# Optimization experiments

Measured on AMD Instinct MI355X. Metric: run time of the kernel, lower is better.

Reference implementation:

```python
import jax, jax.numpy as jnp
import numpy as np


def setup_inputs() -> dict:
    key = jax.random.key(0)
    k1, _ = jax.random.split(key)
    N = 4096
    states = jax.random.normal(k1, (N, 8), dtype=jnp.float32)
    log_tau = jnp.log(jnp.asarray(0.05, dtype=jnp.float32))
    return {"states": states, "log_tau": log_tau}


def reference(states, log_tau):
    N = states.shape[0]
    tau = jnp.exp(log_tau)
    pos = (states[:, :2] + states[:, 2:4]) / 2.0   # [N, 2]
    vel = (states[:, 4:6] + states[:, 6:8]) / 2.0  # [N, 2]
    dpos = pos[:, None, :] - pos[None, :, :]       # [N, N, 2]
    dvel = vel[:, None, :] - vel[None, :, :]       # [N, N, 2]
    f_ij = jnp.concatenate([dpos, dvel], axis=-1)  # [N, N, 4]
    dist = jnp.sqrt(jnp.sum(dpos ** 2, axis=-1) + 1e-08)  # [N, N]
    eye = jnp.eye(N, dtype=bool)
    logits = jnp.where(eye, -1e9, -dist / tau)
    alpha = jax.nn.softmax(logits, axis=-1)        # [N, N]
    mu = jnp.einsum('ij,ijd->id', alpha, f_ij)     # [N, 4]
    diff2 = (f_ij - mu[:, None, :]) ** 2           # [N, N, 4]
    sigma = jnp.sqrt(jnp.einsum('ij,ijd->id', alpha, diff2) + 1e-06)  # [N, 4]
    group_vel = jnp.broadcast_to(jnp.mean(vel, axis=0, keepdims=True), (N, 2))
    vel_dev = vel - group_vel
    return jnp.concatenate([mu, sigma, group_vel, vel_dev], axis=-1)  # [N, 12]
```

## Files before the change

### kernel.cpp

```cpp
#include <hip/hip_runtime.h>
#include <math.h>

typedef float v2f __attribute__((ext_vector_type(2)));

#define N_PTS 4096
#define BLOCK 512
#define RPB 4
#define SLICES (BLOCK / RPB)
#define JPS (N_PTS / SLICES)

__global__ __launch_bounds__(BLOCK, 4) void fused_kernel(
        const float* __restrict__ states,
        const float* __restrict__ log_tau_p,
        float* __restrict__ out) {
    __shared__ float4 pv[N_PTS];
    __shared__ float wsum[8][2];
    __shared__ float red[8][RPB][10];

    const int tid  = threadIdx.x;
    const int lane = tid & 63;
    const int wave = tid >> 6;

    const float c = -__expf(-log_tau_p[0]) * 1.4426950408889634f;

    float svx = 0.f, svy = 0.f;
    #pragma unroll
    for (int k = 0; k < N_PTS / BLOCK; ++k) {
        const int p = tid + k * BLOCK;
        const float4 s0 = *reinterpret_cast<const float4*>(states + p * 8);
        const float4 s1 = *reinterpret_cast<const float4*>(states + p * 8 + 4);
        float4 e;
        e.x = (s0.x + s0.z) * 0.5f;
        e.y = (s0.y + s0.w) * 0.5f;
        e.z = (s1.x + s1.z) * 0.5f;
        e.w = (s1.y + s1.w) * 0.5f;
        pv[p] = e;
        svx += e.z; svy += e.w;
    }
    #pragma unroll
    for (int off = 32; off; off >>= 1) {
        svx += __shfl_down(svx, off);
        svy += __shfl_down(svy, off);
    }
    if (lane == 0) { wsum[wave][0] = svx; wsum[wave][1] = svy; }
    __syncthreads();

    const int rowg  = blockIdx.x * RPB + (lane & 3);
    const int slice = wave * (SLICES / 8) + (lane >> 2);
    const float4 pi = pv[rowg];

    float l = 0.f;
    v2f S1p = {0.f, 0.f}, S1v = {0.f, 0.f}, S2p = {0.f, 0.f}, S2v = {0.f, 0.f};

    #pragma unroll 8
    for (int tt = 0; tt < JPS; ++tt) {
        const float4 q = pv[slice + tt * SLICES];
        v2f dp = {pi.x - q.x, pi.y - q.y};
        v2f dv = {pi.z - q.z, pi.w - q.w};
        v2f p2 = dp * dp;
        float d2 = p2.x + p2.y + 1e-8f;
        float dist = __builtin_amdgcn_sqrtf(d2);
        float w = __builtin_amdgcn_exp2f(dist * c);
        l += w;
        v2f wv = {w, w};
        S1p += dp * wv;
        S1v += dv * wv;
        S2p += p2 * wv;
        S2v += (dv * dv) * wv;
    }

    #pragma unroll
    for (int off = 4; off < 64; off <<= 1) {
        l     += __shfl_xor(l, off);
        S1p.x += __shfl_xor(S1p.x, off);
        S1p.y += __shfl_xor(S1p.y, off);
        S1v.x += __shfl_xor(S1v.x, off);
        S1v.y += __shfl_xor(S1v.y, off);
        S2p.x += __shfl_xor(S2p.x, off);
        S2p.y += __shfl_xor(S2p.y, off);
        S2v.x += __shfl_xor(S2v.x, off);
        S2v.y += __shfl_xor(S2v.y, off);
    }
    if (lane < RPB) {
        float* rr = red[wave][lane];
        rr[0] = l;
        rr[1] = S1p.x; rr[2] = S1p.y; rr[3] = S1v.x; rr[4] = S1v.y;
        rr[5] = S2p.x; rr[6] = S2p.y; rr[7] = S2v.x; rr[8] = S2v.y;
    }
    __syncthreads();

    if (tid < RPB) {
        float acc[9];
        #pragma unroll
        for (int cc = 0; cc < 9; ++cc) acc[cc] = red[0][tid][cc];
        #pragma unroll
        for (int wv = 1; wv < 8; ++wv)
            #pragma unroll
            for (int cc = 0; cc < 9; ++cc) acc[cc] += red[wv][tid][cc];

        const float w_diag = __builtin_amdgcn_exp2f(__builtin_amdgcn_sqrtf(1e-8f) * c);
        const float inv_l = 1.0f / (acc[0] - w_diag);

        float gvx = 0.f, gvy = 0.f;
        #pragma unroll
        for (int wv = 0; wv < 8; ++wv) { gvx += wsum[wv][0]; gvy += wsum[wv][1]; }
        gvx *= (1.0f / N_PTS);
        gvy *= (1.0f / N_PTS);

        const int row = blockIdx.x * RPB + tid;
        const float4 pr = pv[row];

        float mu[4], sg[4];
        #pragma unroll
        for (int d = 0; d < 4; ++d) mu[d] = acc[1 + d] * inv_l;
        #pragma unroll
        for (int d = 0; d < 4; ++d) {
            float v = fmaf(-mu[d], mu[d], acc[5 + d] * inv_l);
            sg[d] = __builtin_amdgcn_sqrtf(v + 1e-6f);
        }
        float4* o = reinterpret_cast<float4*>(out + row * 12);
        o[0] = make_float4(mu[0], mu[1], mu[2], mu[3]);
        o[1] = make_float4(sg[0], sg[1], sg[2], sg[3]);
        o[2] = make_float4(gvx, gvy, pr.z - gvx, pr.w - gvy);
    }
}

extern "C" void kernel_launch(void* const* d_in, const int* in_sizes, int n_in,
                              void* d_out, int out_size, void* d_ws, size_t ws_size,
                              hipStream_t stream) {
    const float* states  = (const float*)d_in[0];
    const float* log_tau = (const float*)d_in[1];
    float* out = (float*)d_out;
    fused_kernel<<<N_PTS / RPB, BLOCK, 0, stream>>>(states, log_tau, out);
}
```

Before: 69.99 us.

## Stage points in two LDS chunks and prescale positions to cut per-pair ops

Shared memory is halved by loading the point table in two 2048-point chunks with a sync between passes, and launch bounds rise from 4 to 6 blocks per CU to allow more resident blocks. Positions are prescaled by 1/tau*log2e so the inner loop drops the multiply before exp2. The squared terms now reuse the weighted products, and the results are rescaled once at the end. This adds extra barriers and a second staging pass per block, and it changes rounding slightly.

```diff
diff --git a/kernel.cpp b/kernel.cpp
--- a/kernel.cpp
+++ b/kernel.cpp
@@ -6,14 +6,16 @@
 #define N_PTS 4096
 #define BLOCK 512
 #define RPB 4
+#define CHUNK 2048
 #define SLICES (BLOCK / RPB)
-#define JPS (N_PTS / SLICES)
+#define JPS (CHUNK / SLICES)
+#define PPT (CHUNK / BLOCK)
 
-__global__ __launch_bounds__(BLOCK, 4) void fused_kernel(
+__global__ __launch_bounds__(BLOCK, 6) void fused_kernel(
         const float* __restrict__ states,
         const float* __restrict__ log_tau_p,
         float* __restrict__ out) {
-    __shared__ float4 pv[N_PTS];
+    __shared__ float4 pvs[CHUNK];
     __shared__ float wsum[8][2];
     __shared__ float red[8][RPB][10];
 
@@ -21,53 +23,64 @@
     const int lane = tid & 63;
     const int wave = tid >> 6;
 
-    const float c = -__expf(-log_tau_p[0]) * 1.4426950408889634f;
+    const float s    = __expf(-log_tau_p[0]) * 1.4426950408889634f;
+    const float eps2 = 1e-8f * s * s;
 
-    float svx = 0.f, svy = 0.f;
+    const int rowg = blockIdx.x * RPB + (lane & 3);
+    const float4 r0 = *reinterpret_cast<const float4*>(states + rowg * 8);
+    const float4 r1 = *reinterpret_cast<const float4*>(states + rowg * 8 + 4);
+    const v2f pis = { (r0.x + r0.z) * 0.5f * s, (r0.y + r0.w) * 0.5f * s };
+    const v2f piv = { (r1.x + r1.z) * 0.5f,     (r1.y + r1.w) * 0.5f };
+
+    const int slice = wave * (SLICES / 8) + (lane >> 2);
+
+    float l = 0.f, svx = 0.f, svy = 0.f;
+    v2f S1p = {0.f, 0.f}, S1v = {0.f, 0.f}, S2p = {0.f, 0.f}, S2v = {0.f, 0.f};
+
     #pragma unroll
-    for (int k = 0; k < N_PTS / BLOCK; ++k) {
-        const int p = tid + k * BLOCK;
-        const float4 s0 = *reinterpret_cast<const float4*>(states + p * 8);
-        const float4 s1 = *reinterpret_cast<const float4*>(states + p * 8 + 4);
-        float4 e;
-        e.x = (s0.x + s0.z) * 0.5f;
-        e.y = (s0.y + s0.w) * 0.5f;
-        e.z = (s1.x + s1.z) * 0.5f;
-        e.w = (s1.y + s1.w) * 0.5f;
-        pv[p] = e;
-        svx += e.z; svy += e.w;
+    for (int pass = 0; pass < N_PTS / CHUNK; ++pass) {
+        const int J0 = pass * CHUNK;
+        #pragma unroll
+        for (int k = 0; k < PPT; ++k) {
+            const int p = tid + k * BLOCK;
+            const float4 s0 = *reinterpret_cast<const float4*>(states + (J0 + p) * 8);
+            const float4 s1 = *reinterpret_cast<const float4*>(states + (J0 + p) * 8 + 4);
+            float4 e;
+            e.x = (s0.x + s0.z) * 0.5f * s;
+            e.y = (s0.y + s0.w) * 0.5f * s;
+            e.z = (s1.x + s1.z) * 0.5f;
+            e.w = (s1.y + s1.w) * 0.5f;
+            pvs[p] = e;
+            svx += e.z; svy += e.w;
+        }
+        __syncthreads();
+
+        #pragma unroll 8
+        for (int tt = 0; tt < JPS; ++tt) {
+            const float4 q = pvs[slice + tt * SLICES];
+            v2f dp = { pis.x - q.x, pis.y - q.y };
+            v2f dv = { piv.x - q.z, piv.y - q.w };
+            float d2 = fmaf(dp.x, dp.x, fmaf(dp.y, dp.y, eps2));
+            float w  = __builtin_amdgcn_exp2f(-__builtin_amdgcn_sqrtf(d2));
+            l += w;
+            v2f wv = { w, w };
+            v2f t0 = dp * wv;
+            v2f t1 = dv * wv;
+            S1p += t0;
+            S1v += t1;
+            S2p += t0 * dp;
+            S2v += t1 * dv;
+        }
+        __syncthreads();
     }
+
+    float tx = svx, ty = svy;
     #pragma unroll
     for (int off = 32; off; off >>= 1) {
-        svx += __shfl_down(svx, off);
-        svy += __shfl_down(svy, off);
+        tx += __shfl_down(tx, off);
+        ty += __shfl_down(ty, off);
     }
-    if (lane == 0) { wsum[wave][0] = svx; wsum[wave][1] = svy; }
-    __syncthreads();
-
-    const int rowg  = blockIdx.x * RPB + (lane & 3);
-    const int slice = wave * (SLICES / 8) + (lane >> 2);
-    const float4 pi = pv[rowg];
-
-    float l = 0.f;
-    v2f S1p = {0.f, 0.f}, S1v = {0.f, 0.f}, S2p = {0.f, 0.f}, S2v = {0.f, 0.f};
-
-    #pragma unroll 8
-    for (int tt = 0; tt < JPS; ++tt) {
-        const float4 q = pv[slice + tt * SLICES];
-        v2f dp = {pi.x - q.x, pi.y - q.y};
-        v2f dv = {pi.z - q.z, pi.w - q.w};
-        v2f p2 = dp * dp;
-        float d2 = p2.x + p2.y + 1e-8f;
-        float dist = __builtin_amdgcn_sqrtf(d2);
-        float w = __builtin_amdgcn_exp2f(dist * c);
-        l += w;
-        v2f wv = {w, w};
-        S1p += dp * wv;
-        S1v += dv * wv;
-        S2p += p2 * wv;
-        S2v += (dv * dv) * wv;
-    }
+    if (lane == 0) { wsum[wave][0] = tx; wsum[wave][1] = ty; }
 
     #pragma unroll
     for (int off = 4; off < 64; off <<= 1) {
@@ -98,8 +111,9 @@
             #pragma unroll
             for (int cc = 0; cc < 9; ++cc) acc[cc] += red[wv][tid][cc];
 
-        const float w_diag = __builtin_amdgcn_exp2f(__builtin_amdgcn_sqrtf(1e-8f) * c);
+        const float w_diag = __builtin_amdgcn_exp2f(-__builtin_amdgcn_sqrtf(eps2));
         const float inv_l = 1.0f / (acc[0] - w_diag);
+        const float inv_s = 1.0f / s;
 
         float gvx = 0.f, gvy = 0.f;
         #pragma unroll
@@ -108,20 +122,29 @@
         gvy *= (1.0f / N_PTS);
 
         const int row = blockIdx.x * RPB + tid;
-        const float4 pr = pv[row];
+        const float4 q1 = *reinterpret_cast<const float4*>(states + row * 8 + 4);
+        const float rvx = (q1.x + q1.z) * 0.5f;
+        const float rvy = (q1.y + q1.w) * 0.5f;
 
         float mu[4], sg[4];
+        mu[0] = acc[1] * inv_l * inv_s;
+        mu[1] = acc[2] * inv_l * inv_s;
+        mu[2] = acc[3] * inv_l;
+        mu[3] = acc[4] * inv_l;
+        const float inv_s2 = inv_s * inv_s;
+        float e2[4];
+        e2[0] = acc[5] * inv_l * inv_s2;
+        e2[1] = acc[6] * inv_l * inv_s2;
+        e2[2] = acc[7] * inv_l;
+        e2[3] = acc[8] * inv_l;
         #pragma unroll
-        for (int d = 0; d < 4; ++d) mu[d] = acc[1 + d] * inv_l;
-        #pragma unroll
-        for (int d = 0; d < 4; ++d) {
-            float v = fmaf(-mu[d], mu[d], acc[5 + d] * inv_l);
-            sg[d] = __builtin_amdgcn_sqrtf(v + 1e-6f);
-        }
+        for (int d = 0; d < 4; ++d)
+            sg[d] = __builtin_amdgcn_sqrtf(fmaf(-mu[d], mu[d], e2[d]) + 1e-6f);
+
         float4* o = reinterpret_cast<float4*>(out + row * 12);
         o[0] = make_float4(mu[0], mu[1], mu[2], mu[3]);
         o[1] = make_float4(sg[0], sg[1], sg[2], sg[3]);
-        o[2] = make_float4(gvx, gvy, pr.z - gvx, pr.w - gvy);
+        o[2] = make_float4(gvx, gvy, rvx - gvx, rvy - gvy);
     }
 }
 
```

Result: no change. 70.32 us (+0.5%).
